# Performance work log

Measured on AMD Instinct MI355X. Metric: run time of the kernel, lower is better.

## Reference

```python
import jax, jax.numpy as jnp
import numpy as np

# dims
T, B, C_IN, C_OUT, NE, RD = 256, 8, 256, 256, 64, 64
TAU = 1.0          # gumbel_tau
COMMIT = 0.25      # commitment_scale
KMEANS = 1.0       # train_embeddings_scale
IMP = 30.0         # imp_loss_scale (hard-coded in module)


def setup_inputs() -> dict:
    key = jax.random.key(0)
    k0, k1, k2, k3 = jax.random.split(key, 4)
    a = np.sqrt(6.0) / (C_IN + C_OUT)  # dynamic_init_method==1 uniform bound
    return {
        "x": jax.random.normal(k0, (T, B, C_IN), jnp.float32),
        "map_w": jax.random.normal(k1, (RD, C_IN), jnp.float32) / np.sqrt(C_IN),
        "map_b": jnp.zeros((RD,), jnp.float32),
        "centroids": jax.random.normal(k2, (NE, RD), jnp.float32) * 0.5,
        "pw_w": jax.random.uniform(k3, (NE, C_OUT * C_IN), jnp.float32, -a, a),
        "pw_B": jnp.zeros((1, 1, C_OUT), jnp.float32),
    }


def reference(x, map_w, map_b, centroids, pw_w, pw_B):
    # key projection: (T*B, RD)
    k = x.reshape(T * B, C_IN) @ map_w.T + map_b
    # squared euclidean distances to centroids: (T*B, NE)
    d = (jnp.sum(k * k, axis=1, keepdims=True)
         + jnp.sum(centroids * centroids, axis=1)
         - 2.0 * (k @ centroids.T))
    # gumbel-softmax (soft, training path) with fixed noise
    g = jax.random.gumbel(jax.random.key(42), d.shape, d.dtype)
    resp = jax.nn.softmax((-d + g) / TAU, axis=-1)  # (T*B, NE)
    quantized = resp @ centroids                    # (T*B, RD)
    commitment_loss = jnp.mean((k - jax.lax.stop_gradient(quantized)) ** 2)
    kmeans_loss = jnp.mean((jax.lax.stop_gradient(k) - quantized) ** 2)
    importance = resp.sum(axis=0)                   # (NE,)
    imp_loss = jnp.std(importance, ddof=1) / jnp.mean(importance)
    loss = COMMIT * commitment_loss + IMP * imp_loss + KMEANS * kmeans_loss
    # soft expert-weight combine then per-token matvec
    w = (resp @ pw_w).reshape(T, B, C_OUT, C_IN)    # (T,B,out,in)
    out = jnp.einsum('tboi,tbi->tbo', w, x) + pw_B  # constant-bias mode
    return out, loss
```

## Files before the change

kernel.cpp:

```cpp
#include <hip/hip_runtime.h>
#include <stdint.h>

#define CIN   256
#define COUT  256
#define NE    64
#define RD    64
#define NTOK  2048

typedef __attribute__((ext_vector_type(8))) short bf16x8;
typedef __attribute__((ext_vector_type(4))) float f32x4;

__device__ inline unsigned short f2bf(float f) {
    uint32_t u = __float_as_uint(f);
    uint32_t r = (u + 0x7FFFu + ((u >> 16) & 1u)) >> 16;
    return (unsigned short)r;
}

__device__ inline float wave_sum(float v) {
    #pragma unroll
    for (int m = 1; m < 64; m <<= 1) v += __shfl_xor(v, m, 64);
    return v;
}
__device__ inline float wave_max(float v) {
    #pragma unroll
    for (int m = 1; m < 64; m <<= 1) v = fmaxf(v, __shfl_xor(v, m, 64));
    return v;
}

__device__ inline uint32_t rotl32(uint32_t v, int d) { return (v << d) | (v >> (32 - d)); }

__device__ inline void threefry_0_42(uint32_t c0, uint32_t c1, uint32_t& o0, uint32_t& o1) {
    const uint32_t ks0 = 0u, ks1 = 42u, ks2 = 0u ^ 42u ^ 0x1BD11BDAu;
    uint32_t x0 = c0 + ks0, x1 = c1 + ks1;
#define TF_R(r) { x0 += x1; x1 = rotl32(x1, r); x1 ^= x0; }
    TF_R(13) TF_R(15) TF_R(26) TF_R(6)
    x0 += ks1; x1 += ks2 + 1u;
    TF_R(17) TF_R(29) TF_R(16) TF_R(24)
    x0 += ks2; x1 += ks0 + 2u;
    TF_R(13) TF_R(15) TF_R(26) TF_R(6)
    x0 += ks0; x1 += ks1 + 3u;
    TF_R(17) TF_R(29) TF_R(16) TF_R(24)
    x0 += ks1; x1 += ks2 + 4u;
    TF_R(13) TF_R(15) TF_R(26) TF_R(6)
    x0 += ks2; x1 += ks0 + 5u;
#undef TF_R
    o0 = x0; o1 = x1;
}

__global__ __launch_bounds__(256) void vq_pack_kernel(
    const float* __restrict__ pw, unsigned short* __restrict__ Bp,
    const float* __restrict__ x, const float* __restrict__ mw,
    const float* __restrict__ mb, const float* __restrict__ cent,
    float* __restrict__ resp_out, float* __restrict__ commit_out)
{
    __shared__ float xs[4][CIN];
    __shared__ float cs[NE][RD + 1];
    __shared__ float ksh[4][RD];
    __shared__ float rs[4][NE];

    const int tid = threadIdx.x;

    if (blockIdx.x >= 512) {
        int G = (blockIdx.x - 512) * 256 + tid;
        int tile = G >> 8, qg = G & 255;
        int ct = tile >> 9, g = (tile >> 6) & 7, p = tile & 63;
        int e = (g << 3) + (p >> 3), kc = p & 7;
        int n = qg >> 2, gp = qg & 3;
        int k16 = gp ^ ((n >> 1) & 3);
        int o = (ct << 6) + n;
        const float* s = pw + ((size_t)e << 16) + (o << 8) + (kc << 5) + (k16 << 3);
        float4 v0 = *(const float4*)s;
        float4 v1 = *(const float4*)(s + 4);
        ushort4 a, b;
        a.x = f2bf(v0.x); a.y = f2bf(v0.y); a.z = f2bf(v0.z); a.w = f2bf(v0.w);
        b.x = f2bf(v1.x); b.y = f2bf(v1.y); b.z = f2bf(v1.z); b.w = f2bf(v1.w);
        *(ushort4*)(Bp + ((size_t)G << 3)) = a;
        *(ushort4*)(Bp + ((size_t)G << 3) + 4) = b;
        return;
    }

    const int w  = tid >> 6;
    const int t  = tid & 63;
    const int tb = (blockIdx.x << 2) + w;

    ((float4*)xs[w])[t] = ((const float4*)(x + (size_t)tb * CIN))[t];
    #pragma unroll
    for (int j = 0; j < 4; ++j) {
        int fidx = (j << 8) + tid;
        float4 v = ((const float4*)cent)[fidx];
        int row = fidx >> 4, c0 = (fidx & 15) << 2;
        cs[row][c0] = v.x; cs[row][c0 + 1] = v.y; cs[row][c0 + 2] = v.z; cs[row][c0 + 3] = v.w;
    }
    __syncthreads();

    float kr = mb[t];
    const float4* mwr = (const float4*)(mw + (size_t)t * CIN);
    #pragma unroll 8
    for (int j = 0; j < 64; ++j) {
        float4 wv = mwr[j];
        kr += wv.x * xs[w][(j << 2)] + wv.y * xs[w][(j << 2) + 1]
            + wv.z * xs[w][(j << 2) + 2] + wv.w * xs[w][(j << 2) + 3];
    }
    ksh[w][t] = kr;
    float kk = wave_sum(kr * kr);
    __syncthreads();

    float cc = 0.f, dt = 0.f;
    #pragma unroll 8
    for (int r = 0; r < 64; ++r) {
        float cv = cs[t][r];
        cc += cv * cv;
        dt += ksh[w][r] * cv;
    }
    float d = kk + cc - 2.f * dt;

    uint32_t fidx = (uint32_t)((tb << 6) + t);
    uint32_t cnt  = fidx < 65536u ? fidx : fidx - 65536u;
    uint32_t o0, o1;
    threefry_0_42(cnt, cnt + 65536u, o0, o1);
    uint32_t bits = fidx < 65536u ? o0 : o1;
    float uf = __uint_as_float((bits >> 9) | 0x3f800000u) - 1.0f;
    uf = fmaxf(uf, 1.17549435e-38f);
    float g2 = -logf(-logf(uf));

    float sv = g2 - d;
    float mx = wave_max(sv);
    float pz = expf(sv - mx);
    float ps = wave_sum(pz);
    float rv = pz / ps;
    resp_out[(tb << 6) + t] = rv;
    rs[w][t] = rv;
    __syncthreads();

    float q = 0.f;
    #pragma unroll 8
    for (int e2 = 0; e2 < 64; ++e2) q += rs[w][e2] * cs[e2][t];
    float df = kr - q;
    float sq = wave_sum(df * df);
    if (t == 0) commit_out[tb] = sq;
}

struct GemmRegs {
    f32x4 P00, P01, P02, P03, P10, P11, P12, P13;
    f32x4 O00, O01, O02, O03, O10, O11, O12, O13;
};

template<int T>
__device__ __attribute__((always_inline)) inline void stage16(
    const char* bsrc, char* Bb, int w, int lane)
{
    const char* src = bsrc + ((size_t)T << 14) + (w << 12) + (lane << 4);
    char* dst = Bb + ((T & 3) << 14) + (w << 12);
    #pragma unroll
    for (int i = 0; i < 4; ++i)
        __builtin_amdgcn_global_load_lds(
            (const __attribute__((address_space(1))) unsigned int*)(src + (i << 10)),
            (__attribute__((address_space(3))) unsigned int*)(dst + (i << 10)), 16, 0, 0);
}

template<int T>
__device__ __attribute__((always_inline)) inline void phase(
    const char* bsrc, char* Bb,
    const bf16x8& a00, const bf16x8& a01, const bf16x8& a02, const bf16x8& a03,
    const bf16x8& a10, const bf16x8& a11, const bf16x8& a12, const bf16x8& a13,
    GemmRegs& R, const float (*rsh)[8], int w, int lane, int lo, int kq)
{
    if constexpr (T <= 13)      asm volatile("s_waitcnt vmcnt(8)" ::: "memory");
    else if constexpr (T == 14) asm volatile("s_waitcnt vmcnt(4)" ::: "memory");
    else                        asm volatile("s_waitcnt vmcnt(0)" ::: "memory");
    asm volatile("s_barrier" ::: "memory");

    if constexpr (T + 3 < 16) stage16<T + 3>(bsrc, Bb, w, lane);

    const char* bt = Bb + ((T & 3) << 14);
    #pragma unroll
    for (int kc = 0; kc < 4; ++kc) {
        const char* bk = bt + (kc << 12);
        bf16x8 b0, b1, b2, b3;
        { int n = lo;      b0 = *(const bf16x8*)(bk + (n << 6) + ((kq ^ ((n >> 1) & 3)) << 4)); }
        { int n = 16 + lo; b1 = *(const bf16x8*)(bk + (n << 6) + ((kq ^ ((n >> 1) & 3)) << 4)); }
        { int n = 32 + lo; b2 = *(const bf16x8*)(bk + (n << 6) + ((kq ^ ((n >> 1) & 3)) << 4)); }
        { int n = 48 + lo; b3 = *(const bf16x8*)(bk + (n << 6) + ((kq ^ ((n >> 1) & 3)) << 4)); }
        const bf16x8& am0 = (kc == 0) ? a00 : (kc == 1) ? a01 : (kc == 2) ? a02 : a03;
        const bf16x8& am1 = (kc == 0) ? a10 : (kc == 1) ? a11 : (kc == 2) ? a12 : a13;
        R.P00 = __builtin_amdgcn_mfma_f32_16x16x32_bf16(am0, b0, R.P00, 0, 0, 0);
        R.P01 = __builtin_amdgcn_mfma_f32_16x16x32_bf16(am0, b1, R.P01, 0, 0, 0);
        R.P02 = __builtin_amdgcn_mfma_f32_16x16x32_bf16(am0, b2, R.P02, 0, 0, 0);
        R.P03 = __builtin_amdgcn_mfma_f32_16x16x32_bf16(am0, b3, R.P03, 0, 0, 0);
        R.P10 = __builtin_amdgcn_mfma_f32_16x16x32_bf16(am1, b0, R.P10, 0, 0, 0);
        R.P11 = __builtin_amdgcn_mfma_f32_16x16x32_bf16(am1, b1, R.P11, 0, 0, 0);
        R.P12 = __builtin_amdgcn_mfma_f32_16x16x32_bf16(am1, b2, R.P12, 0, 0, 0);
        R.P13 = __builtin_amdgcn_mfma_f32_16x16x32_bf16(am1, b3, R.P13, 0, 0, 0);
    }

    if constexpr (T & 1) {
        constexpr int el = T >> 1;
        const int rb = (w << 5) + (kq << 2);
        float r00 = rsh[rb +  0][el], r01 = rsh[rb +  1][el];
        float r02 = rsh[rb +  2][el], r03 = rsh[rb +  3][el];
        float r10 = rsh[rb + 16][el], r11 = rsh[rb + 17][el];
        float r12 = rsh[rb + 18][el], r13 = rsh[rb + 19][el];
        const f32x4 z = {};
        R.O00[0] += r00 * R.P00[0]; R.O00[1] += r01 * R.P00[1]; R.O00[2] += r02 * R.P00[2]; R.O00[3] += r03 * R.P00[3];
        R.O01[0] += r00 * R.P01[0]; R.O01[1] += r01 * R.P01[1]; R.O01[2] += r02 * R.P01[2]; R.O01[3] += r03 * R.P01[3];
        R.O02[0] += r00 * R.P02[0]; R.O02[1] += r01 * R.P02[1]; R.O02[2] += r02 * R.P02[2]; R.O02[3] += r03 * R.P02[3];
        R.O03[0] += r00 * R.P03[0]; R.O03[1] += r01 * R.P03[1]; R.O03[2] += r02 * R.P03[2]; R.O03[3] += r03 * R.P03[3];
        R.O10[0] += r10 * R.P10[0]; R.O10[1] += r11 * R.P10[1]; R.O10[2] += r12 * R.P10[2]; R.O10[3] += r13 * R.P10[3];
        R.O11[0] += r10 * R.P11[0]; R.O11[1] += r11 * R.P11[1]; R.O11[2] += r12 * R.P11[2]; R.O11[3] += r13 * R.P11[3];
        R.O12[0] += r10 * R.P12[0]; R.O12[1] += r11 * R.P12[1]; R.O12[2] += r12 * R.P12[2]; R.O12[3] += r13 * R.P12[3];
        R.O13[0] += r10 * R.P13[0]; R.O13[1] += r11 * R.P13[1]; R.O13[2] += r12 * R.P13[2]; R.O13[3] += r13 * R.P13[3];
        R.P00 = z; R.P01 = z; R.P02 = z; R.P03 = z;
        R.P10 = z; R.P11 = z; R.P12 = z; R.P13 = z;
    }
}

#define LOAD_AF(name, base, idx) { \
    const float* s_ = (base) + ((idx) << 5); \
    float4 v0_ = *(const float4*)s_; \
    float4 v1_ = *(const float4*)(s_ + 4); \
    bf16x8 bv_; \
    bv_[0] = (short)f2bf(v0_.x); bv_[1] = (short)f2bf(v0_.y); \
    bv_[2] = (short)f2bf(v0_.z); bv_[3] = (short)f2bf(v0_.w); \
    bv_[4] = (short)f2bf(v1_.x); bv_[5] = (short)f2bf(v1_.y); \
    bv_[6] = (short)f2bf(v1_.z); bv_[7] = (short)f2bf(v1_.w); \
    name = bv_; }

__global__ __launch_bounds__(256, 2) void gemm_kernel(
    const float* __restrict__ x, const float* __restrict__ resp,
    const unsigned short* __restrict__ Bp, float* __restrict__ partial)
{
    __shared__ char Bb[65536];
    __shared__ float rsh[128][8];

    const int tid  = threadIdx.x;
    const int lane = tid & 63;
    const int w    = tid >> 6;
    const int lo   = lane & 15, kq = lane >> 4;
    const int bid  = blockIdx.x;
    const int g    = bid & 7, ct = (bid >> 3) & 3, mt = bid >> 5;
    const int m0   = mt << 7;

    {
        int idx = tid << 2;
        int row = idx >> 3, e0 = idx & 7;
        float4 rv = *(const float4*)(resp + ((size_t)(m0 + row) << 6) + (g << 3) + e0);
        *(float4*)(&rsh[row][e0]) = rv;
    }

    bf16x8 af00, af01, af02, af03, af04, af05, af06, af07;
    bf16x8 af10, af11, af12, af13, af14, af15, af16, af17;
    {
        const float* xb0 = x + ((size_t)(m0 + (w << 5) + lo) << 8) + (kq << 3);
        const float* xb1 = xb0 + (16 << 8);
        LOAD_AF(af00, xb0, 0) LOAD_AF(af01, xb0, 1) LOAD_AF(af02, xb0, 2) LOAD_AF(af03, xb0, 3)
        LOAD_AF(af04, xb0, 4) LOAD_AF(af05, xb0, 5) LOAD_AF(af06, xb0, 6) LOAD_AF(af07, xb0, 7)
        LOAD_AF(af10, xb1, 0) LOAD_AF(af11, xb1, 1) LOAD_AF(af12, xb1, 2) LOAD_AF(af13, xb1, 3)
        LOAD_AF(af14, xb1, 4) LOAD_AF(af15, xb1, 5) LOAD_AF(af16, xb1, 6) LOAD_AF(af17, xb1, 7)
    }

    const char* bsrc = (const char*)Bp + ((size_t)((ct << 3) + g) << 18);

    asm volatile("s_waitcnt vmcnt(0)" ::: "memory");
    asm volatile("s_waitcnt lgkmcnt(0)" ::: "memory");

    stage16<0>(bsrc, Bb, w, lane);
    stage16<1>(bsrc, Bb, w, lane);
    stage16<2>(bsrc, Bb, w, lane);

    GemmRegs R = {};

    phase< 0>(bsrc, Bb, af00, af01, af02, af03, af10, af11, af12, af13, R, rsh, w, lane, lo, kq);
    phase< 1>(bsrc, Bb, af04, af05, af06, af07, af14, af15, af16, af17, R, rsh, w, lane, lo, kq);
    phase< 2>(bsrc, Bb, af00, af01, af02, af03, af10, af11, af12, af13, R, rsh, w, lane, lo, kq);
    phase< 3>(bsrc, Bb, af04, af05, af06, af07, af14, af15, af16, af17, R, rsh, w, lane, lo, kq);
    phase< 4>(bsrc, Bb, af00, af01, af02, af03, af10, af11, af12, af13, R, rsh, w, lane, lo, kq);
    phase< 5>(bsrc, Bb, af04, af05, af06, af07, af14, af15, af16, af17, R, rsh, w, lane, lo, kq);
    phase< 6>(bsrc, Bb, af00, af01, af02, af03, af10, af11, af12, af13, R, rsh, w, lane, lo, kq);
    phase< 7>(bsrc, Bb, af04, af05, af06, af07, af14, af15, af16, af17, R, rsh, w, lane, lo, kq);
    phase< 8>(bsrc, Bb, af00, af01, af02, af03, af10, af11, af12, af13, R, rsh, w, lane, lo, kq);
    phase< 9>(bsrc, Bb, af04, af05, af06, af07, af14, af15, af16, af17, R, rsh, w, lane, lo, kq);
    phase<10>(bsrc, Bb, af00, af01, af02, af03, af10, af11, af12, af13, R, rsh, w, lane, lo, kq);
    phase<11>(bsrc, Bb, af04, af05, af06, af07, af14, af15, af16, af17, R, rsh, w, lane, lo, kq);
    phase<12>(bsrc, Bb, af00, af01, af02, af03, af10, af11, af12, af13, R, rsh, w, lane, lo, kq);
    phase<13>(bsrc, Bb, af04, af05, af06, af07, af14, af15, af16, af17, R, rsh, w, lane, lo, kq);
    phase<14>(bsrc, Bb, af00, af01, af02, af03, af10, af11, af12, af13, R, rsh, w, lane, lo, kq);
    phase<15>(bsrc, Bb, af04, af05, af06, af07, af14, af15, af16, af17, R, rsh, w, lane, lo, kq);

    float* pout = partial + ((size_t)g << 19)
                + ((size_t)(m0 + (w << 5) + (kq << 2)) << 8) + (ct << 6) + lo;
    {
        float* pr;
        pr = pout;                  pr[0] = R.O00[0]; pr[16] = R.O01[0]; pr[32] = R.O02[0]; pr[48] = R.O03[0];
        pr = pout + 256;            pr[0] = R.O00[1]; pr[16] = R.O01[1]; pr[32] = R.O02[1]; pr[48] = R.O03[1];
        pr = pout + 512;            pr[0] = R.O00[2]; pr[16] = R.O01[2]; pr[32] = R.O02[2]; pr[48] = R.O03[2];
        pr = pout + 768;            pr[0] = R.O00[3]; pr[16] = R.O01[3]; pr[32] = R.O02[3]; pr[48] = R.O03[3];
        pr = pout + 4096;           pr[0] = R.O10[0]; pr[16] = R.O11[0]; pr[32] = R.O12[0]; pr[48] = R.O13[0];
        pr = pout + 4096 + 256;     pr[0] = R.O10[1]; pr[16] = R.O11[1]; pr[32] = R.O12[1]; pr[48] = R.O13[1];
        pr = pout + 4096 + 512;     pr[0] = R.O10[2]; pr[16] = R.O11[2]; pr[32] = R.O12[2]; pr[48] = R.O13[2];
        pr = pout + 4096 + 768;     pr[0] = R.O10[3]; pr[16] = R.O11[3]; pr[32] = R.O12[3]; pr[48] = R.O13[3];
    }
}

__global__ __launch_bounds__(256) void reduce_loss_kernel(
    const float* __restrict__ partial, const float* __restrict__ bias,
    float* __restrict__ out, const float* __restrict__ resp,
    const float* __restrict__ commit_part, float* __restrict__ imp_p,
    float* __restrict__ cm_p)
{
    __shared__ float part[4][64];
    const int t = threadIdx.x;

    if (blockIdx.x < 512) {
        int idx = blockIdx.x * 256 + t;
        float4 s = ((const float4*)bias)[idx & 63];
        #pragma unroll
        for (int g = 0; g < 8; ++g) {
            float4 v = ((const float4*)partial)[((size_t)g << 17) + idx];
            s.x += v.x; s.y += v.y; s.z += v.z; s.w += v.w;
        }
        ((float4*)out)[idx] = s;
        return;
    }

    const int b = blockIdx.x - 512;
    const int e = t & 63, grp = t >> 6;
    float s = 0.f;
    #pragma unroll
    for (int j = 0; j < 16; ++j)
        s += resp[(size_t)((b << 6) + (grp << 4) + j) * 64 + e];
    part[grp][e] = s;
    __syncthreads();
    if (t < 64) {
        float v = part[0][t] + part[1][t] + part[2][t] + part[3][t];
        imp_p[(b << 6) + t] = v;
        float cm = commit_part[(b << 6) + t];
        cm = wave_sum(cm);
        if (t == 0) cm_p[b] = cm;
    }
}

__global__ __launch_bounds__(64) void loss_final_kernel(const float* __restrict__ imp_p,
                                                        const float* __restrict__ cm_p,
                                                        float* __restrict__ loss_out)
{
    const int t = threadIdx.x;
    float imp = 0.f;
    #pragma unroll
    for (int b = 0; b < 32; ++b) imp += imp_p[(b << 6) + t];
    float ct = (t < 32) ? cm_p[t] : 0.f;
    ct = wave_sum(ct);
    float tot  = wave_sum(imp);
    float mean = tot * (1.0f / 64.f);
    float dv   = imp - mean;
    float var  = wave_sum(dv * dv) * (1.0f / 63.f);
    if (t == 0) {
        float mse = ct * (1.0f / (float)(NTOK * RD));
        float imp_loss = sqrtf(var) / mean;
        loss_out[0] = (0.25f + 1.0f) * mse + 30.0f * imp_loss;
    }
}

extern "C" void kernel_launch(void* const* d_in, const int* in_sizes, int n_in,
                              void* d_out, int out_size, void* d_ws, size_t ws_size,
                              hipStream_t stream)
{
    const float* x     = (const float*)d_in[0];
    const float* map_w = (const float*)d_in[1];
    const float* map_b = (const float*)d_in[2];
    const float* cent  = (const float*)d_in[3];
    const float* pw_w  = (const float*)d_in[4];
    const float* pw_B  = (const float*)d_in[5];
    float* out = (float*)d_out;

    char* ws = (char*)d_ws;
    float* resp        = (float*)ws;
    float* commit      = (float*)(ws + 524288);
    float* imp_p       = (float*)(ws + 540672);
    float* cm_p        = (float*)(ws + 557056);
    unsigned short* Bp = (unsigned short*)(ws + (1u << 20));
    float* partial     = (float*)(ws + (10u << 20));

    vq_pack_kernel<<<2560, 256, 0, stream>>>(pw_w, Bp, x, map_w, map_b, cent, resp, commit);
    gemm_kernel<<<512, 256, 0, stream>>>(x, resp, Bp, partial);
    reduce_loss_kernel<<<544, 256, 0, stream>>>(partial, pw_B, out, resp, commit, imp_p, cm_p);
    loss_final_kernel<<<1, 64, 0, stream>>>(imp_p, cm_p, out + NTOK * COUT);
}
```

Measured before the change: 57.07 us.

## Shrink GEMM LDS ring to three stages and fold loss kernels into neighbors

The LDS staging ring for the expert-weight B tiles drops from four 16KB buffers to three. Prefetch distance falls from 3 to 2 and the vmcnt waits change to match. This cuts LDS from about 68KB to 52KB per block, which could let more blocks fit per CU, at the cost of less latency hiding per block. The importance/commitment partial reduction moves into extra blocks of the GEMM launch, and the final loss computation moves into one extra block of the output-reduce kernel, removing one kernel launch.

```diff
diff --git a/kernel.cpp b/kernel.cpp
--- a/kernel.cpp
+++ b/kernel.cpp
@@ -150,7 +150,7 @@
     const char* bsrc, char* Bb, int w, int lane)
 {
     const char* src = bsrc + ((size_t)T << 14) + (w << 12) + (lane << 4);
-    char* dst = Bb + ((T & 3) << 14) + (w << 12);
+    char* dst = Bb + (T % 3) * 16384 + (w << 12);
     #pragma unroll
     for (int i = 0; i < 4; ++i)
         __builtin_amdgcn_global_load_lds(
@@ -165,14 +165,13 @@
     const bf16x8& a10, const bf16x8& a11, const bf16x8& a12, const bf16x8& a13,
     GemmRegs& R, const float (*rsh)[8], int w, int lane, int lo, int kq)
 {
-    if constexpr (T <= 13)      asm volatile("s_waitcnt vmcnt(8)" ::: "memory");
-    else if constexpr (T == 14) asm volatile("s_waitcnt vmcnt(4)" ::: "memory");
-    else                        asm volatile("s_waitcnt vmcnt(0)" ::: "memory");
+    if constexpr (T <= 14) asm volatile("s_waitcnt vmcnt(4)" ::: "memory");
+    else                   asm volatile("s_waitcnt vmcnt(0)" ::: "memory");
     asm volatile("s_barrier" ::: "memory");
 
-    if constexpr (T + 3 < 16) stage16<T + 3>(bsrc, Bb, w, lane);
-
-    const char* bt = Bb + ((T & 3) << 14);
+    if constexpr (T + 2 < 16) stage16<T + 2>(bsrc, Bb, w, lane);
+
+    const char* bt = Bb + (T % 3) * 16384;
     #pragma unroll
     for (int kc = 0; kc < 4; ++kc) {
         const char* bk = bt + (kc << 12);
@@ -225,14 +224,37 @@
     bv_[6] = (short)f2bf(v1_.z); bv_[7] = (short)f2bf(v1_.w); \
     name = bv_; }
 
-__global__ __launch_bounds__(256, 2) void gemm_kernel(
+__global__ __launch_bounds__(256, 2) void gemm_loss_kernel(
     const float* __restrict__ x, const float* __restrict__ resp,
-    const unsigned short* __restrict__ Bp, float* __restrict__ partial)
-{
-    __shared__ char Bb[65536];
+    const unsigned short* __restrict__ Bp, float* __restrict__ partial,
+    const float* __restrict__ commit_part, float* __restrict__ imp_p,
+    float* __restrict__ cm_p)
+{
+    __shared__ char Bb[49152];
     __shared__ float rsh[128][8];
 
     const int tid  = threadIdx.x;
+
+    if (blockIdx.x >= 512) {
+        float (*part)[64] = (float (*)[64])Bb;
+        const int b = blockIdx.x - 512;
+        const int e = tid & 63, grp = tid >> 6;
+        float s = 0.f;
+        #pragma unroll
+        for (int j = 0; j < 16; ++j)
+            s += resp[(size_t)((b << 6) + (grp << 4) + j) * 64 + e];
+        part[grp][e] = s;
+        __syncthreads();
+        if (tid < 64) {
+            float v = part[0][tid] + part[1][tid] + part[2][tid] + part[3][tid];
+            imp_p[(b << 6) + tid] = v;
+            float cm = commit_part[(b << 6) + tid];
+            cm = wave_sum(cm);
+            if (tid == 0) cm_p[b] = cm;
+        }
+        return;
+    }
+
     const int lane = tid & 63;
     const int w    = tid >> 6;
     const int lo   = lane & 15, kq = lane >> 4;
@@ -265,7 +287,6 @@
 
     stage16<0>(bsrc, Bb, w, lane);
     stage16<1>(bsrc, Bb, w, lane);
-    stage16<2>(bsrc, Bb, w, lane);
 
     GemmRegs R = {};
 
@@ -301,13 +322,11 @@
     }
 }
 
-__global__ __launch_bounds__(256) void reduce_loss_kernel(
+__global__ __launch_bounds__(256) void reduce_final_kernel(
     const float* __restrict__ partial, const float* __restrict__ bias,
-    float* __restrict__ out, const float* __restrict__ resp,
-    const float* __restrict__ commit_part, float* __restrict__ imp_p,
-    float* __restrict__ cm_p)
-{
-    __shared__ float part[4][64];
+    float* __restrict__ out, const float* __restrict__ imp_p,
+    const float* __restrict__ cm_p, float* __restrict__ loss_out)
+{
     const int t = threadIdx.x;
 
     if (blockIdx.x < 512) {
@@ -322,41 +341,21 @@
         return;
     }
 
-    const int b = blockIdx.x - 512;
-    const int e = t & 63, grp = t >> 6;
-    float s = 0.f;
-    #pragma unroll
-    for (int j = 0; j < 16; ++j)
-        s += resp[(size_t)((b << 6) + (grp << 4) + j) * 64 + e];
-    part[grp][e] = s;
-    __syncthreads();
     if (t < 64) {
-        float v = part[0][t] + part[1][t] + part[2][t] + part[3][t];
-        imp_p[(b << 6) + t] = v;
-        float cm = commit_part[(b << 6) + t];
-        cm = wave_sum(cm);
-        if (t == 0) cm_p[b] = cm;
-    }
-}
-
-__global__ __launch_bounds__(64) void loss_final_kernel(const float* __restrict__ imp_p,
-                                                        const float* __restrict__ cm_p,
-                                                        float* __restrict__ loss_out)
-{
-    const int t = threadIdx.x;
-    float imp = 0.f;
-    #pragma unroll
-    for (int b = 0; b < 32; ++b) imp += imp_p[(b << 6) + t];
-    float ct = (t < 32) ? cm_p[t] : 0.f;
-    ct = wave_sum(ct);
-    float tot  = wave_sum(imp);
-    float mean = tot * (1.0f / 64.f);
-    float dv   = imp - mean;
-    float var  = wave_sum(dv * dv) * (1.0f / 63.f);
-    if (t == 0) {
-        float mse = ct * (1.0f / (float)(NTOK * RD));
-        float imp_loss = sqrtf(var) / mean;
-        loss_out[0] = (0.25f + 1.0f) * mse + 30.0f * imp_loss;
+        float imp = 0.f;
+        #pragma unroll
+        for (int b = 0; b < 32; ++b) imp += imp_p[(b << 6) + t];
+        float ct = (t < 32) ? cm_p[t] : 0.f;
+        ct = wave_sum(ct);
+        float tot  = wave_sum(imp);
+        float mean = tot * (1.0f / 64.f);
+        float dv   = imp - mean;
+        float var  = wave_sum(dv * dv) * (1.0f / 63.f);
+        if (t == 0) {
+            float mse = ct * (1.0f / (float)(NTOK * RD));
+            float imp_loss = sqrtf(var) / mean;
+            loss_out[0] = (0.25f + 1.0f) * mse + 30.0f * imp_loss;
+        }
     }
 }
 
@@ -380,8 +379,10 @@
     unsigned short* Bp = (unsigned short*)(ws + (1u << 20));
     float* partial     = (float*)(ws + (10u << 20));
 
-    vq_pack_kernel<<<2560, 256, 0, stream>>>(pw_w, Bp, x, map_w, map_b, cent, resp, commit);
-    gemm_kernel<<<512, 256, 0, stream>>>(x, resp, Bp, partial);
-    reduce_loss_kernel<<<544, 256, 0, stream>>>(partial, pw_B, out, resp, commit, imp_p, cm_p);
-    loss_final_kernel<<<1, 64, 0, stream>>>(imp_p, cm_p, out + NTOK * COUT);
-}
+    vq_pack_kernel<<<2560, 256, 0, stream>>>(pw_w, Bp, x, map_w, map_b, cent,
+                                             resp, commit);
+    gemm_loss_kernel<<<544, 256, 0, stream>>>(x, resp, Bp, partial,
+                                              commit, imp_p, cm_p);
+    reduce_final_kernel<<<513, 256, 0, stream>>>(partial, pw_B, out,
+                                                 imp_p, cm_p, out + NTOK * COUT);
+}
```

Result: faster. 54.85 us (median of 2 runs) (-3.9%).
